# Performance work log

Measured on AMD Instinct MI355X. Metric: run time of the kernel, lower is better.

Reference implementation:

```python
import jax, jax.numpy as jnp
import numpy as np

NUM_EMBED = 1024
HEAD_SIZE = 64
B, T = 4, 4096

def setup_inputs() -> dict:
    key = jax.random.key(0)
    kx, kq, kk, kv = jax.random.split(key, 4)
    scale = NUM_EMBED ** -0.5
    return {
        "x": jax.random.normal(kx, (B, T, NUM_EMBED), dtype=jnp.float32),
        "Wq": jax.random.normal(kq, (NUM_EMBED, HEAD_SIZE), dtype=jnp.float32) * scale,
        "Wk": jax.random.normal(kk, (NUM_EMBED, HEAD_SIZE), dtype=jnp.float32) * scale,
        "Wv": jax.random.normal(kv, (NUM_EMBED, HEAD_SIZE), dtype=jnp.float32) * scale,
    }

def reference(x, Wq, Wk, Wv):
    # x: [B,T,C]; Wq/Wk/Wv: [C,H]
    q = jnp.einsum('btc,ch->bth', x, Wq)
    k = jnp.einsum('btc,ch->bth', x, Wk)
    v = jnp.einsum('btc,ch->bth', x, Wv)
    Tq = x.shape[1]
    att = jnp.einsum('bth,bsh->bts', q, k) * (k.shape[-1] ** -0.5)  # [B,T,T]
    causal = jnp.tril(jnp.ones((Tq, Tq), dtype=bool))
    att = jnp.where(causal, att, -jnp.inf)
    att = jax.nn.softmax(att, axis=-1)
    # dropout p=0 (eval mode): identity
    out = jnp.einsum('bts,bsh->bth', att, v)  # [B,T,H]
    return out
```

## Files before the change

### kernel.cpp

```cpp
#include <hip/hip_runtime.h>

#define B_ 4
#define T_ 4096
#define C_ 1024
#define H_ 64

typedef _Float16 half8  __attribute__((ext_vector_type(8)));
typedef _Float16 half4_ __attribute__((ext_vector_type(4)));
typedef float    floatx4 __attribute__((ext_vector_type(4)));

#define MFMA16(a, b, c)  __builtin_amdgcn_mfma_f32_16x16x32_f16(a, b, c, 0, 0, 0)
#define MFMA16K(a, b, c) __builtin_amdgcn_mfma_f32_16x16x16f16(a, b, c, 0, 0, 0)
#define LO4(v) __builtin_shufflevector(v, v, 0, 1, 2, 3)
#define HI4(v) __builtin_shufflevector(v, v, 4, 5, 6, 7)

__global__ __launch_bounds__(256) void pack_w_kn(
    const float* __restrict__ Wq, const float* __restrict__ Wk,
    const float* __restrict__ Wv, _Float16* __restrict__ Wt2)
{
    const int idx  = blockIdx.x * 256 + threadIdx.x;
    const int mt   = idx >> 14;
    const int j    = (idx >> 10) & 15;
    const int f    = (idx >> 9) & 1;
    const int lane = (idx >> 3) & 63;
    const int jj   = idx & 7;
    const int q = lane >> 4, c = lane & 15;
    const int k  = j * 64 + f * 32 + q * 8 + jj;
    const int hp = mt * 16 + c;
    const float* W = (hp < 64) ? Wq : (hp < 128) ? Wk : Wv;
    Wt2[idx] = (_Float16)W[k * H_ + (hp & 63)];
}

__global__ __launch_bounds__(512) void qkv_kn(
    const float* __restrict__ x, const _Float16* __restrict__ Wt2,
    _Float16* __restrict__ Qh, _Float16* __restrict__ Kpk,
    _Float16* __restrict__ Vpk)
{
    __shared__ _Float16 xs[2][32][72];
    const int tid  = threadIdx.x;
    const int lane = tid & 63, w = tid >> 6;
    const int q    = lane >> 4, c = lane & 15;
    const int nt   = w & 1;
    const int mg   = w >> 1;
    const int row0 = blockIdx.x * 32;

    const int srow = tid >> 4, scol = (tid & 15) * 4;
    const float* xg = x + (size_t)(row0 + srow) * C_ + scol;

    floatx4 acc[3];
    #pragma unroll
    for (int i = 0; i < 3; ++i) acc[i] = floatx4{0.f, 0.f, 0.f, 0.f};

    float4 g = *(const float4*)xg;

    for (int j = 0; j < 16; ++j) {
        half4_ hv;
        hv[0] = (_Float16)g.x; hv[1] = (_Float16)g.y;
        hv[2] = (_Float16)g.z; hv[3] = (_Float16)g.w;
        *(half4_*)(&xs[j & 1][srow][scol]) = hv;
        __syncthreads();
        if (j < 15) g = *(const float4*)(xg + (j + 1) * 64);

        const _Float16* xrow = &xs[j & 1][nt * 16 + c][q * 8];
        const half8 b0 = *(const half8*)xrow;
        const half8 b1 = *(const half8*)(xrow + 32);

        half8 a[6];
        #pragma unroll
        for (int i = 0; i < 3; ++i) {
            const size_t fb = ((size_t)((mg * 3 + i) * 16 + j) * 2) * 512 + lane * 8;
            a[i * 2]     = *(const half8*)(Wt2 + fb);
            a[i * 2 + 1] = *(const half8*)(Wt2 + fb + 512);
        }
        #pragma unroll
        for (int i = 0; i < 3; ++i) {
            acc[i] = MFMA16(a[i * 2],     b0, acc[i]);
            acc[i] = MFMA16(a[i * 2 + 1], b1, acc[i]);
        }
    }

    const int row = row0 + nt * 16 + c;
    const int b = row >> 12, t4 = row & (T_ - 1);
    const int kt = t4 >> 6;
    const size_t tbase = ((size_t)b * 64 + kt) * 4096;
    const int mtk = (t4 >> 4) & 3;
    const int kk  = t4 & 63;

    #pragma unroll
    for (int i = 0; i < 3; ++i) {
        const int gi = mg * 3 + i;
        if (gi < 4) {
            half4_ v;
            #pragma unroll
            for (int r = 0; r < 4; ++r) v[r] = (_Float16)acc[i][r];
            *(half4_*)(Qh + (size_t)row * H_ + gi * 16 + q * 4) = v;
        } else if (gi < 8) {
            half4_ v;
            #pragma unroll
            for (int r = 0; r < 4; ++r) v[r] = (_Float16)acc[i][r];
            const int e  = gi - 4;
            const int f  = e >> 1;
            const int qa = (e * 2 + (q >> 1)) & 3;
            *(half4_*)(Kpk + tbase + ((size_t)(mtk * 2 + f) * 64 + qa * 16 + c) * 8
                       + (q & 1) * 4) = v;
        } else {
            const int mtv = gi - 8;
            const int qa2 = (kk >> 2) & 3;
            const int h4  = (kk >> 4) & 1;
            const int f2  = kk >> 5;
            const int i2  = kk & 3;
            #pragma unroll
            for (int r = 0; r < 4; ++r) {
                const int cv = q * 4 + r;
                Vpk[tbase + ((size_t)(mtv * 2 + f2) * 64 + qa2 * 16 + cv) * 8
                    + h4 * 4 + i2] = (_Float16)acc[i][r];
            }
        }
    }
}

__global__ __launch_bounds__(512, 4) void attn_kn(
    const _Float16* __restrict__ Qh, const _Float16* __restrict__ Kpk,
    const _Float16* __restrict__ Vpk, float* __restrict__ Opart,
    float* __restrict__ Mp, float* __restrict__ Lp)
{
    __shared__ __align__(16) _Float16 KVs[2][2][4096];
    const int tid  = threadIdx.x;
    const int lane = tid & 63;
    const int w    = tid >> 6;
    const int q    = lane >> 4, c = lane & 15;

    const int bid  = blockIdx.x;
    const int xcd  = bid & 7;
    const int slot = bid >> 3;
    const int b    = xcd >> 1;
    const int tau  = 31 - (slot >> 2);
    const int s    = ((slot & 3) << 1) | (xcd & 1);
    const int row0 = tau * 128;
    const int wrow0 = row0 + w * 16;
    const int nk_blk = 2 * tau + 2;
    const int nk_w   = (wrow0 >> 6) + 1;
    const int ntb = (s < nk_blk) ? (((nk_blk - 1 - s) >> 3) + 1) : 0;

    const _Float16* qb = Qh + (size_t)(b * T_ + wrow0 + c) * H_;
    half8 bq0 = *(const half8*)(qb + q * 8);
    half8 bq1 = *(const half8*)(qb + 32 + q * 8);
    const _Float16 qs = (_Float16)0.18033688f;
    bq0 *= qs; bq1 *= qs;

    floatx4 o[4];
    #pragma unroll
    for (int i = 0; i < 4; ++i) o[i] = floatx4{0.f, 0.f, 0.f, 0.f};
    float m = -3.0e38f, l = 0.f;

    const _Float16* Kb = Kpk + (size_t)b * 262144;
    const _Float16* Vb = Vpk + (size_t)b * 262144;

    if (ntb > 0) {
        const _Float16* Kt = Kb + (size_t)s * 4096;
        const _Float16* Vt = Vb + (size_t)s * 4096;
        *(half8*)(&KVs[0][0][tid * 8]) = *(const half8*)(Kt + tid * 8);
        *(half8*)(&KVs[0][1][tid * 8]) = *(const half8*)(Vt + tid * 8);
    }
    __syncthreads();

    #pragma unroll 1
    for (int i = 0; i < ntb; ++i) {
        const int kt = s + 8 * i;
        const bool more = (i + 1 < ntb);
        half8 gk, gv;
        if (more) {
            const _Float16* Kt = Kb + (size_t)(kt + 8) * 4096;
            const _Float16* Vt = Vb + (size_t)(kt + 8) * 4096;
            gk = *(const half8*)(Kt + tid * 8);
            gv = *(const half8*)(Vt + tid * 8);
        }

        if (kt < nk_w) {
            const _Float16* Ks = &KVs[i & 1][0][0];
            const _Float16* Vs = &KVs[i & 1][1][0];

            floatx4 sS[4];
            __builtin_amdgcn_s_setprio(1);
            #pragma unroll
            for (int mt = 0; mt < 4; ++mt) {
                const half8 ka = *(const half8*)(Ks + ((mt * 2)     * 64 + lane) * 8);
                const half8 kb2= *(const half8*)(Ks + ((mt * 2 + 1) * 64 + lane) * 8);
                floatx4 z = floatx4{0.f, 0.f, 0.f, 0.f};
                z = MFMA16(ka, bq0, z);
                sS[mt] = MFMA16(kb2, bq1, z);
            }
            __builtin_amdgcn_s_setprio(0);

            if (kt == nk_w - 1) {
                const int kb0 = kt * 64;
                #pragma unroll
                for (int mt = 0; mt < 4; ++mt)
                    #pragma unroll
                    for (int r = 0; r < 4; ++r)
                        if (kb0 + mt * 16 + q * 4 + r > wrow0 + c)
                            sS[mt][r] = -3.0e38f;
            }

            float mx = sS[0][0];
            #pragma unroll
            for (int mt = 0; mt < 4; ++mt)
                #pragma unroll
                for (int r = 0; r < 4; ++r) mx = fmaxf(mx, sS[mt][r]);
            mx = fmaxf(mx, __shfl_xor(mx, 16, 64));
            mx = fmaxf(mx, __shfl_xor(mx, 32, 64));
            if (!__all(mx <= m + 8.f)) {
                const float mn    = fmaxf(m, mx);
                const float alpha = exp2f(m - mn);
                l *= alpha;
                #pragma unroll
                for (int mt = 0; mt < 4; ++mt) o[mt] *= alpha;
                m = mn;
            }
            half4_ ph[4];
            float sl = 0.f;
            #pragma unroll
            for (int mt = 0; mt < 4; ++mt)
                #pragma unroll
                for (int r = 0; r < 4; ++r) {
                    const float ev = exp2f(sS[mt][r] - m);
                    sl += ev;
                    ph[mt][r] = (_Float16)ev;
                }
            sl += __shfl_xor(sl, 16, 64);
            sl += __shfl_xor(sl, 32, 64);
            l += sl;

            __builtin_amdgcn_s_setprio(1);
            #pragma unroll
            for (int mt = 0; mt < 4; ++mt) {
                const half8 va = *(const half8*)(Vs + ((mt * 2)     * 64 + lane) * 8);
                const half8 vb = *(const half8*)(Vs + ((mt * 2 + 1) * 64 + lane) * 8);
                o[mt] = MFMA16K(LO4(va), ph[0], o[mt]);
                o[mt] = MFMA16K(HI4(va), ph[1], o[mt]);
                o[mt] = MFMA16K(LO4(vb), ph[2], o[mt]);
                o[mt] = MFMA16K(HI4(vb), ph[3], o[mt]);
            }
            __builtin_amdgcn_s_setprio(0);
        }

        __syncthreads();
        if (more) {
            *(half8*)(&KVs[(i + 1) & 1][0][tid * 8]) = gk;
            *(half8*)(&KVs[(i + 1) & 1][1][tid * 8]) = gv;
            __syncthreads();
        }
    }

    float* Ob = Opart + ((size_t)bid * 8 + w) * 1024;
    #pragma unroll
    for (int mt = 0; mt < 4; ++mt)
        *(floatx4*)(Ob + mt * 256 + lane * 4) = o[mt];
    if (q == 0) {
        Mp[(size_t)bid * 128 + w * 16 + c] = m;
        Lp[(size_t)bid * 128 + w * 16 + c] = l;
    }
}

__global__ __launch_bounds__(64) void combine_kn(
    const float* __restrict__ Opart, const float* __restrict__ Mp,
    const float* __restrict__ Lp, float* __restrict__ out)
{
    __shared__ float sO[64][17];
    const int cb  = blockIdx.x;
    const int w2  = cb & 7;
    const int tau = (cb >> 3) & 31;
    const int b   = cb >> 8;
    const int lane = threadIdx.x;
    const int q = lane >> 4, c = lane & 15;

    int items[8];
    #pragma unroll
    for (int s = 0; s < 8; ++s) {
        const int xcd  = b * 2 + (s & 1);
        const int slot = (31 - tau) * 4 + (s >> 1);
        items[s] = slot * 8 + xcd;
    }

    float Mv[8], Lv[8];
    #pragma unroll
    for (int s = 0; s < 8; ++s) {
        Mv[s] = Mp[(size_t)items[s] * 128 + w2 * 16 + c];
        Lv[s] = Lp[(size_t)items[s] * 128 + w2 * 16 + c];
    }
    float M = Mv[0];
    #pragma unroll
    for (int s = 1; s < 8; ++s) M = fmaxf(M, Mv[s]);
    float L = 0.f;
    float a[8];
    #pragma unroll
    for (int s = 0; s < 8; ++s) {
        a[s] = exp2f(Mv[s] - M);
        L += Lv[s] * a[s];
    }
    const float inv = 1.f / L;

    floatx4 acc[4];
    #pragma unroll
    for (int mt = 0; mt < 4; ++mt) acc[mt] = floatx4{0.f, 0.f, 0.f, 0.f};
    #pragma unroll
    for (int s = 0; s < 8; ++s) {
        const float* Ob = Opart + ((size_t)items[s] * 8 + w2) * 1024;
        #pragma unroll
        for (int mt = 0; mt < 4; ++mt) {
            const floatx4 v = *(const floatx4*)(Ob + mt * 256 + lane * 4);
            acc[mt] += v * a[s];
        }
    }
    #pragma unroll
    for (int mt = 0; mt < 4; ++mt)
        #pragma unroll
        for (int r = 0; r < 4; ++r)
            sO[mt * 16 + q * 4 + r][c] = acc[mt][r] * inv;
    __syncthreads();

    const int orow = lane >> 2;
    const int seg  = lane & 3;
    float* dst = out + (size_t)(b * T_ + tau * 128 + w2 * 16 + orow) * H_ + seg * 16;
    #pragma unroll
    for (int v4 = 0; v4 < 4; ++v4) {
        float4 vv;
        vv.x = sO[seg * 16 + v4 * 4 + 0][orow];
        vv.y = sO[seg * 16 + v4 * 4 + 1][orow];
        vv.z = sO[seg * 16 + v4 * 4 + 2][orow];
        vv.w = sO[seg * 16 + v4 * 4 + 3][orow];
        *(float4*)(dst + v4 * 4) = vv;
    }
}

extern "C" void kernel_launch(void* const* d_in, const int* in_sizes, int n_in,
                              void* d_out, int out_size, void* d_ws, size_t ws_size,
                              hipStream_t stream) {
    const float* x  = (const float*)d_in[0];
    const float* Wq = (const float*)d_in[1];
    const float* Wk = (const float*)d_in[2];
    const float* Wv = (const float*)d_in[3];
    float* out = (float*)d_out;

    _Float16* ws = (_Float16*)d_ws;
    _Float16* Wt2 = ws;
    _Float16* Qh  = ws + 196608;
    _Float16* Kpk = Qh + 1048576;
    _Float16* Vpk = Kpk + 1048576;
    float* Opart = (float*)(ws + 3342336);
    float* Mp    = Opart + 8388608;
    float* Lp    = Mp + 131072;

    hipLaunchKernelGGL(pack_w_kn, dim3(768), dim3(256), 0, stream, Wq, Wk, Wv, Wt2);
    hipLaunchKernelGGL(qkv_kn, dim3((B_ * T_) / 32), dim3(512), 0, stream,
                       x, Wt2, Qh, Kpk, Vpk);
    hipLaunchKernelGGL(attn_kn, dim3(1024), dim3(512), 0, stream,
                       Qh, Kpk, Vpk, Opart, Mp, Lp);
    hipLaunchKernelGGL(combine_kn, dim3(1024), dim3(64), 0, stream,
                       Opart, Mp, Lp, out);
}
```

Before: 142.0 us.

## Fuse split-K combine into attention kernel via last-block atomic counter

```diff
diff --git a/kernel.cpp b/kernel.cpp
--- a/kernel.cpp
+++ b/kernel.cpp
@@ -16,8 +16,10 @@
 
 __global__ __launch_bounds__(256) void pack_w_kn(
     const float* __restrict__ Wq, const float* __restrict__ Wk,
-    const float* __restrict__ Wv, _Float16* __restrict__ Wt2)
+    const float* __restrict__ Wv, _Float16* __restrict__ Wt2,
+    int* __restrict__ tick)
 {
+    if (blockIdx.x == 0 && threadIdx.x < 128) tick[threadIdx.x] = 0;
     const int idx  = blockIdx.x * 256 + threadIdx.x;
     const int mt   = idx >> 14;
     const int j    = (idx >> 10) & 15;
@@ -122,9 +124,12 @@
 __global__ __launch_bounds__(512, 4) void attn_kn(
     const _Float16* __restrict__ Qh, const _Float16* __restrict__ Kpk,
     const _Float16* __restrict__ Vpk, float* __restrict__ Opart,
-    float* __restrict__ Mp, float* __restrict__ Lp)
+    float* __restrict__ Mp, float* __restrict__ Lp, int* __restrict__ tick,
+    float* __restrict__ out)
 {
-    __shared__ __align__(16) _Float16 KVs[2][2][4096];
+    __shared__ __align__(16) char smem[36864];
+    __shared__ int s_last;
+    _Float16 (*KVs)[2][4096] = (_Float16 (*)[2][4096])smem;
     const int tid  = threadIdx.x;
     const int lane = tid & 63;
     const int w    = tid >> 6;
@@ -260,75 +265,72 @@
         Mp[(size_t)bid * 128 + w * 16 + c] = m;
         Lp[(size_t)bid * 128 + w * 16 + c] = l;
     }
-}
-
-__global__ __launch_bounds__(64) void combine_kn(
-    const float* __restrict__ Opart, const float* __restrict__ Mp,
-    const float* __restrict__ Lp, float* __restrict__ out)
-{
-    __shared__ float sO[64][17];
-    const int cb  = blockIdx.x;
-    const int w2  = cb & 7;
-    const int tau = (cb >> 3) & 31;
-    const int b   = cb >> 8;
-    const int lane = threadIdx.x;
-    const int q = lane >> 4, c = lane & 15;
+
+    __syncthreads();
+    if (tid == 0) {
+        __threadfence();
+        s_last = atomicAdd(&tick[b * 32 + tau], 1);
+    }
+    __syncthreads();
+    if (s_last != 7) return;
+    __threadfence();
 
     int items[8];
     #pragma unroll
-    for (int s = 0; s < 8; ++s) {
-        const int xcd  = b * 2 + (s & 1);
-        const int slot = (31 - tau) * 4 + (s >> 1);
-        items[s] = slot * 8 + xcd;
-    }
-
+    for (int s2 = 0; s2 < 8; ++s2) {
+        const int x2  = b * 2 + (s2 & 1);
+        const int sl2 = (31 - tau) * 4 + (s2 >> 1);
+        items[s2] = sl2 * 8 + x2;
+    }
     float Mv[8], Lv[8];
     #pragma unroll
-    for (int s = 0; s < 8; ++s) {
-        Mv[s] = Mp[(size_t)items[s] * 128 + w2 * 16 + c];
-        Lv[s] = Lp[(size_t)items[s] * 128 + w2 * 16 + c];
-    }
-    float M = Mv[0];
-    #pragma unroll
-    for (int s = 1; s < 8; ++s) M = fmaxf(M, Mv[s]);
-    float L = 0.f;
-    float a[8];
-    #pragma unroll
-    for (int s = 0; s < 8; ++s) {
-        a[s] = exp2f(Mv[s] - M);
-        L += Lv[s] * a[s];
-    }
-    const float inv = 1.f / L;
+    for (int s2 = 0; s2 < 8; ++s2) {
+        Mv[s2] = Mp[(size_t)items[s2] * 128 + w * 16 + c];
+        Lv[s2] = Lp[(size_t)items[s2] * 128 + w * 16 + c];
+    }
+    float M2 = Mv[0];
+    #pragma unroll
+    for (int s2 = 1; s2 < 8; ++s2) M2 = fmaxf(M2, Mv[s2]);
+    float L2 = 0.f;
+    float a2[8];
+    #pragma unroll
+    for (int s2 = 0; s2 < 8; ++s2) {
+        a2[s2] = exp2f(Mv[s2] - M2);
+        L2 += Lv[s2] * a2[s2];
+    }
+    const float inv = 1.f / L2;
 
     floatx4 acc[4];
     #pragma unroll
     for (int mt = 0; mt < 4; ++mt) acc[mt] = floatx4{0.f, 0.f, 0.f, 0.f};
     #pragma unroll
-    for (int s = 0; s < 8; ++s) {
-        const float* Ob = Opart + ((size_t)items[s] * 8 + w2) * 1024;
+    for (int s2 = 0; s2 < 8; ++s2) {
+        const float* Ob2 = Opart + ((size_t)items[s2] * 8 + w) * 1024;
         #pragma unroll
         for (int mt = 0; mt < 4; ++mt) {
-            const floatx4 v = *(const floatx4*)(Ob + mt * 256 + lane * 4);
-            acc[mt] += v * a[s];
-        }
-    }
+            const floatx4 v = *(const floatx4*)(Ob2 + mt * 256 + lane * 4);
+            acc[mt] += v * a2[s2];
+        }
+    }
+
+    float* sO = (float*)smem + w * 1088;
     #pragma unroll
     for (int mt = 0; mt < 4; ++mt)
         #pragma unroll
         for (int r = 0; r < 4; ++r)
-            sO[mt * 16 + q * 4 + r][c] = acc[mt][r] * inv;
+            sO[(mt * 16 + q * 4 + r) * 17 + c] = acc[mt][r] * inv;
     __syncthreads();
 
     const int orow = lane >> 2;
     const int seg  = lane & 3;
-    float* dst = out + (size_t)(b * T_ + tau * 128 + w2 * 16 + orow) * H_ + seg * 16;
+    float* dst = out + (size_t)(b * T_ + tau * 128 + w * 16 + orow) * H_ + seg * 16;
     #pragma unroll
     for (int v4 = 0; v4 < 4; ++v4) {
         float4 vv;
-        vv.x = sO[seg * 16 + v4 * 4 + 0][orow];
-        vv.y = sO[seg * 16 + v4 * 4 + 1][orow];
-        vv.z = sO[seg * 16 + v4 * 4 + 2][orow];
-        vv.w = sO[seg * 16 + v4 * 4 + 3][orow];
+        vv.x = sO[(seg * 16 + v4 * 4 + 0) * 17 + orow];
+        vv.y = sO[(seg * 16 + v4 * 4 + 1) * 17 + orow];
+        vv.z = sO[(seg * 16 + v4 * 4 + 2) * 17 + orow];
+        vv.w = sO[(seg * 16 + v4 * 4 + 3) * 17 + orow];
         *(float4*)(dst + v4 * 4) = vv;
     }
 }
@@ -350,12 +352,12 @@
     float* Opart = (float*)(ws + 3342336);
     float* Mp    = Opart + 8388608;
     float* Lp    = Mp + 131072;
-
-    hipLaunchKernelGGL(pack_w_kn, dim3(768), dim3(256), 0, stream, Wq, Wk, Wv, Wt2);
+    int*   tick  = (int*)(Lp + 131072);
+
+    hipLaunchKernelGGL(pack_w_kn, dim3(768), dim3(256), 0, stream,
+                       Wq, Wk, Wv, Wt2, tick);
     hipLaunchKernelGGL(qkv_kn, dim3((B_ * T_) / 32), dim3(512), 0, stream,
                        x, Wt2, Qh, Kpk, Vpk);
     hipLaunchKernelGGL(attn_kn, dim3(1024), dim3(512), 0, stream,
-                       Qh, Kpk, Vpk, Opart, Mp, Lp);
-    hipLaunchKernelGGL(combine_kn, dim3(1024), dim3(64), 0, stream,
-                       Opart, Mp, Lp, out);
+                       Qh, Kpk, Vpk, Opart, Mp, Lp, tick, out);
 }
```

New measurement: 236.0 us. 66.2% more time.
